# Kernel tuning notes

Hardware: AMD Instinct MI355X
Metric: run time of the kernel (lower is better)

The kernel has to match this reference:

```python
import jax, jax.numpy as jnp
import numpy as np

B, G, D, N_HEADS, FFN, L = 16, 2048, 256, 8, 1024, 4
HEAD_DIM = D // N_HEADS
EPS_LN = 1e-5
MASK_TOKEN = -10.0
REE_BASE = 100.0


def setup_inputs() -> dict:
    key = jax.random.key(0)
    ks = jax.random.split(key, 20)
    s = 0.02
    inp = {
        'x': jax.random.normal(ks[0], (B, G), jnp.float32),
        'gene_emb': jax.random.normal(ks[1], (G, D), jnp.float32) * s,
        'inv_freq': (1.0 / REE_BASE ** (jnp.arange(0, D, 2, dtype=jnp.float32) / D)),
        'Wq': jax.random.normal(ks[2], (L, D, D), jnp.float32) * s,
        'bq': jnp.zeros((L, D), jnp.float32),
        'Wk': jax.random.normal(ks[3], (L, D, D), jnp.float32) * s,
        'bk': jnp.zeros((L, D), jnp.float32),
        'Wv': jax.random.normal(ks[4], (L, D, D), jnp.float32) * s,
        'bv': jnp.zeros((L, D), jnp.float32),
        'ln1_g': jnp.ones((L, D), jnp.float32),
        'ln1_b': jnp.zeros((L, D), jnp.float32),
        'ln2_g': jnp.ones((L, D), jnp.float32),
        'ln2_b': jnp.zeros((L, D), jnp.float32),
        'WU': jax.random.normal(ks[5], (L, D, FFN), jnp.float32) * s,
        'bU': jnp.zeros((L, FFN), jnp.float32),
        'WV': jax.random.normal(ks[6], (L, FFN, D), jnp.float32) * s,
        'bV': jnp.zeros((L, D), jnp.float32),
        'Wout': jax.random.normal(ks[7], (D, 1), jnp.float32) * s,
        'bout': jnp.zeros((1,), jnp.float32),
    }
    return inp


def layernorm(x, g, b):
    m = x.mean(-1, keepdims=True)
    v = ((x - m) ** 2).mean(-1, keepdims=True)
    return (x - m) / jnp.sqrt(v + EPS_LN) * g + b


def causal_linear_attention(q, k, v):
    # q, k already feature-mapped ('sqr'); shapes [B, S, H, dh]
    b, s, h, dh = q.shape
    qs, ks_, vs = (jnp.moveaxis(t, 1, 0) for t in (q, k, v))  # [S,B,H,dh]
    num0 = jnp.zeros((b, h, dh, dh), q.dtype)
    den0 = jnp.zeros((b, h, dh), q.dtype)

    def step(carry, qkv):
        num_s, den_s = carry
        qt, kt, vt = qkv
        num_s = num_s + jnp.einsum('bhf,bhd->bhfd', kt, vt)
        den_s = den_s + kt
        num = jnp.einsum('bhf,bhfd->bhd', qt, num_s)
        den = jnp.einsum('bhf,bhf->bh', qt, den_s)
        return (num_s, den_s), num / (den[..., None] + 1e-16)

    _, out = jax.lax.scan(step, (num0, den0), (qs, ks_, vs))  # [S,B,H,dh]
    return jnp.moveaxis(out, 0, 1).reshape(b, s, h * dh)


def reference(x, gene_emb, inv_freq, Wq, bq, Wk, bk, Wv, bv,
              ln1_g, ln1_b, ln2_g, ln2_b, WU, bU, WV, bV, Wout, bout):
    b, g = x.shape
    # Rotary Expression Embedding
    freqs = x[..., None] * inv_freq  # [B,G,D/2]
    emb = jnp.concatenate([jnp.sin(freqs), jnp.cos(freqs)], axis=-1)  # [B,G,D]
    emb = jnp.where((x == MASK_TOKEN)[..., None], 0.0, emb)
    h = gene_emb[None] + emb  # [B,G,D]

    for l in range(Wq.shape[0]):
        hn = layernorm(h, ln1_g[l], ln1_b[l])  # pre-LN (on_gptln=True)
        q = (hn @ Wq[l] + bq[l]).reshape(b, g, N_HEADS, HEAD_DIM) ** 2
        k = (hn @ Wk[l] + bk[l]).reshape(b, g, N_HEADS, HEAD_DIM) ** 2
        v = (hn @ Wv[l] + bv[l]).reshape(b, g, N_HEADS, HEAD_DIM)
        h = h + causal_linear_attention(q, k, v)
        hn2 = layernorm(h, ln2_g[l], ln2_b[l])
        h = h + jax.nn.gelu(hn2 @ WU[l] + bU[l], approximate=False) @ WV[l] + bV[l]
    return (h @ Wout + bout).squeeze(-1)  # [B,G]
```

## Files before the change

kernel.cpp:

```cpp
#include <hip/hip_runtime.h>
#include <math.h>


#define GG 2048
#define DD 256
#define NROWS 32768
#define NC 32
#define CS 64

typedef __attribute__((ext_vector_type(8))) short bf16x8;
typedef __attribute__((ext_vector_type(4))) float f32x4;

__device__ __forceinline__ short f2bf(float f) {
  union { float f; unsigned u; } v; v.f = f;
  unsigned r = v.u + 0x7FFFu + ((v.u >> 16) & 1u);
  return (short)(r >> 16);
}
__device__ __forceinline__ float bf2f(short s) {
  union { unsigned u; float f; } v; v.u = ((unsigned)(unsigned short)s) << 16;
  return v.f;
}
__device__ __forceinline__ void gld16(const short* g, short* l) {
  __builtin_amdgcn_global_load_lds(
      (const __attribute__((address_space(1))) void*)g,
      (__attribute__((address_space(3))) void*)l, 16, 0, 0);
}
__device__ __forceinline__ float fast_gelu(float x) {
  float y = 1.595769122f * (x + 0.044715f * x * x * x);
  return x / (1.0f + __expf(-y));
}

__global__ __launch_bounds__(256) void embed_kernel(
    const float* __restrict__ x, const float* __restrict__ ge,
    const float* __restrict__ invf, float* __restrict__ h) {
  int bg = blockIdx.x * 4 + (threadIdx.x >> 6);
  int g = bg & (GG - 1);
  int lane = threadIdx.x & 63;
  float xv = x[bg];
  int d = lane * 4;
  float4 e;
  if (lane < 32) {
    float4 f = *(const float4*)&invf[d];
    e.x = sinf(xv * f.x); e.y = sinf(xv * f.y);
    e.z = sinf(xv * f.z); e.w = sinf(xv * f.w);
  } else {
    float4 f = *(const float4*)&invf[d - 128];
    e.x = cosf(xv * f.x); e.y = cosf(xv * f.y);
    e.z = cosf(xv * f.z); e.w = cosf(xv * f.w);
  }
  if (xv == -10.0f) { e.x = 0.f; e.y = 0.f; e.z = 0.f; e.w = 0.f; }
  float4 gv = *(const float4*)&ge[(size_t)g * DD + d];
  float4 o; o.x = gv.x + e.x; o.y = gv.y + e.y; o.z = gv.z + e.z; o.w = gv.w + e.w;
  *(float4*)&h[(size_t)bg * DD + d] = o;
}

__global__ __launch_bounds__(256) void ln_tiled(
    const float* __restrict__ h, const float* __restrict__ gamma,
    const float* __restrict__ beta, short* __restrict__ outT) {
  __shared__ float mean_s[32], rstd_s[32];
  __shared__ float gls[256], bls[256];
  int r0 = blockIdx.x * 32;
  int tid = threadIdx.x;
  gls[tid] = gamma[tid]; bls[tid] = beta[tid];
  {
    int row = tid >> 3, seg = tid & 7;
    const float4* hp = (const float4*)(h + (size_t)(r0 + row) * DD + seg * 32);
    float s = 0.f, s2 = 0.f;
#pragma unroll
    for (int i = 0; i < 8; ++i) {
      float4 v = hp[i];
      s += v.x + v.y + v.z + v.w;
      s2 += v.x * v.x + v.y * v.y + v.z * v.z + v.w * v.w;
    }
    s += __shfl_xor(s, 1); s += __shfl_xor(s, 2); s += __shfl_xor(s, 4);
    s2 += __shfl_xor(s2, 1); s2 += __shfl_xor(s2, 2); s2 += __shfl_xor(s2, 4);
    if (seg == 0) {
      float mn = s * (1.0f / 256.0f);
      mean_s[row] = mn;
      rstd_s[row] = rsqrtf(s2 * (1.0f / 256.0f) - mn * mn + 1e-5f);
    }
  }
  __syncthreads();
  int row = tid & 31, kc8 = (tid >> 5) & 3, half = tid >> 7;
  float mn = mean_s[row], rs = rstd_s[row];
  size_t hrow = (size_t)(r0 + row) * DD;
  int trow = (r0 & 127) + row;
  short* tb = outT + (size_t)(r0 >> 7) * 8 * 4096 + (kc8 * 128 + trow) * 8;
#pragma unroll
  for (int j = 0; j < 4; ++j) {
    int kb = half * 4 + j;
    int k0 = kb * 32 + kc8 * 8;
    float4 x0 = *(const float4*)&h[hrow + k0];
    float4 x1 = *(const float4*)&h[hrow + k0 + 4];
    float4 g0 = *(const float4*)&gls[k0], g1 = *(const float4*)&gls[k0 + 4];
    float4 b0 = *(const float4*)&bls[k0], b1 = *(const float4*)&bls[k0 + 4];
    bf16x8 aw;
    aw[0] = f2bf((x0.x - mn) * rs * g0.x + b0.x);
    aw[1] = f2bf((x0.y - mn) * rs * g0.y + b0.y);
    aw[2] = f2bf((x0.z - mn) * rs * g0.z + b0.z);
    aw[3] = f2bf((x0.w - mn) * rs * g0.w + b0.w);
    aw[4] = f2bf((x1.x - mn) * rs * g1.x + b1.x);
    aw[5] = f2bf((x1.y - mn) * rs * g1.y + b1.y);
    aw[6] = f2bf((x1.z - mn) * rs * g1.z + b1.z);
    aw[7] = f2bf((x1.w - mn) * rs * g1.w + b1.w);
    *(bf16x8*)&tb[(size_t)kb * 4096] = aw;
  }
}

__global__ __launch_bounds__(256) void prep_weights(
    const float* __restrict__ Wq, const float* __restrict__ Wk,
    const float* __restrict__ Wv, const float* __restrict__ WU,
    const float* __restrict__ WV,
    short* __restrict__ TQ, short* __restrict__ TK, short* __restrict__ TV,
    short* __restrict__ TU, short* __restrict__ TVd) {
  int zz = blockIdx.z, l = blockIdx.y;
  const float* src; short* dst; int Kd, Nd;
  if (zz == 0) { src = Wq; dst = TQ; Kd = 256; Nd = 256; }
  else if (zz == 1) { src = Wk; dst = TK; Kd = 256; Nd = 256; }
  else if (zz == 2) { src = Wv; dst = TV; Kd = 256; Nd = 256; }
  else if (zz == 3) { src = WU; dst = TU; Kd = 256; Nd = 1024; }
  else { src = WV; dst = TVd; Kd = 1024; Nd = 256; }
  int tot = Kd * Nd;
  int e = blockIdx.x * 256 + threadIdx.x;
  if (e >= tot) return;
  int t = e >> 12;
  int cslot = (e >> 3) & 511;
  int elem = e & 7;
  int kc8 = cslot >> 7, rn = cslot & 127;
  int nKb = Kd >> 5;
  int nt = t / nKb, kb = t - nt * nKb;
  int n = nt * 128 + rn, k = kb * 32 + kc8 * 8 + elem;
  dst[(size_t)l * tot + e] = f2bf(src[(size_t)l * tot + (size_t)k * Nd + n]);
}

template <int K, int EPI>
__global__ __launch_bounds__(256) void gemm_t(
    const short* __restrict__ A, const short* __restrict__ B0,
    const short* __restrict__ B1, const short* __restrict__ B2,
    const float* __restrict__ bias0, const float* __restrict__ bias1,
    const float* __restrict__ bias2,
    short* __restrict__ o0, short* __restrict__ o1, short* __restrict__ o2,
    float* __restrict__ outf, int N) {
  __shared__ __align__(16) short L[24576];
  constexpr int nIter = K / 32;
  int z = blockIdx.z;
  const short* Bt = (z == 0) ? B0 : (z == 1) ? B1 : B2;
  const float* bias = (z == 0) ? bias0 : (z == 1) ? bias1 : bias2;
  short* outz = (z == 0) ? o0 : (z == 1) ? o1 : o2;
  int m0 = blockIdx.x * 128, n0 = blockIdx.y * 128;
  int tid = threadIdx.x;
  int lane = tid & 63, w = tid >> 6;
  int q = lane >> 4, r = lane & 15;
  int wm = (w >> 1) * 64, wn = (w & 1) * 64;
  const short* At = A + (size_t)blockIdx.x * nIter * 4096;
  const short* Btl = Bt + (size_t)blockIdx.y * nIter * 4096;
  f32x4 vzero = {0.f, 0.f, 0.f, 0.f};
  f32x4 acc[4][4];
#pragma unroll
  for (int i = 0; i < 4; ++i)
#pragma unroll
    for (int j = 0; j < 4; ++j) acc[i][j] = vzero;

  int c0 = tid * 8, c1 = (tid + 256) * 8;
#pragma unroll
  for (int g = 0; g < 3; ++g) {
    gld16(At + g * 4096 + c0, &L[g * 4096 + c0]);
    gld16(At + g * 4096 + c1, &L[g * 4096 + c1]);
    gld16(Btl + g * 4096 + c0, &L[12288 + g * 4096 + c0]);
    gld16(Btl + g * 4096 + c1, &L[12288 + g * 4096 + c1]);
  }

  int abase = (q * 128 + wm + r) * 8;
  int bbase = (q * 128 + wn + r) * 8;

#pragma unroll
  for (int gi = 0; gi < nIter; ++gi) {
    const int rem = nIter - 1 - gi;
    if (rem >= 2)      __builtin_amdgcn_s_waitcnt(0x0f78);
    else if (rem == 1) __builtin_amdgcn_s_waitcnt(0x0f74);
    else               __builtin_amdgcn_s_waitcnt(0x0f70);
    __builtin_amdgcn_s_barrier();
    const int cur = gi % 3;
    const short* Asc = &L[cur * 4096];
    const short* Bsc = &L[12288 + cur * 4096];
    bf16x8 af[4], bfr[4];
#pragma unroll
    for (int mt = 0; mt < 4; ++mt)
      af[mt] = *(const bf16x8*)&Asc[abase + mt * 16 * 8];
#pragma unroll
    for (int nt = 0; nt < 4; ++nt)
      bfr[nt] = *(const bf16x8*)&Bsc[bbase + nt * 16 * 8];
#pragma unroll
    for (int mt = 0; mt < 4; ++mt)
#pragma unroll
      for (int nt = 0; nt < 4; ++nt)
        acc[mt][nt] = __builtin_amdgcn_mfma_f32_16x16x32_bf16(bfr[nt], af[mt], acc[mt][nt], 0, 0, 0);
    __builtin_amdgcn_s_waitcnt(0xc07f);
    __builtin_amdgcn_s_barrier();
    if (gi + 3 < nIter) {
      size_t kn = (size_t)(gi + 3) * 4096;
      gld16(At + kn + c0, &L[cur * 4096 + c0]);
      gld16(At + kn + c1, &L[cur * 4096 + c1]);
      gld16(Btl + kn + c0, &L[12288 + cur * 4096 + c0]);
      gld16(Btl + kn + c1, &L[12288 + cur * 4096 + c1]);
    }
  }

  float4 bias4[4];
#pragma unroll
  for (int nt = 0; nt < 4; ++nt) bias4[nt] = *(const float4*)&bias[n0 + wn + nt * 16 + q * 4];

  if (EPI == 0) {
    short* T = L;
#pragma unroll
    for (int mt = 0; mt < 4; ++mt) {
      int ml = wm + mt * 16 + r;
#pragma unroll
      for (int nt = 0; nt < 4; ++nt) {
        f32x4 v = acc[mt][nt];
        v[0] += bias4[nt].x; v[1] += bias4[nt].y; v[2] += bias4[nt].z; v[3] += bias4[nt].w;
        if (z < 2) { v[0] *= v[0]; v[1] *= v[1]; v[2] *= v[2]; v[3] *= v[3]; }
        short4 pk; pk.x = f2bf(v[0]); pk.y = f2bf(v[1]); pk.z = f2bf(v[2]); pk.w = f2bf(v[3]);
        *(short4*)&T[ml * 132 + wn + nt * 16 + q * 4] = pk;
      }
    }
    __syncthreads();
#pragma unroll
    for (int t2 = 0; t2 < 2; ++t2) {
      int task = tid + t2 * 256;
      int row = task & 127, hl = task >> 7;
      size_t obase = ((size_t)((n0 >> 5) + hl) * NROWS + m0 + row) * 32;
#pragma unroll
      for (int j = 0; j < 4; ++j)
        *(bf16x8*)&outz[obase + j * 8] = *(const bf16x8*)&T[row * 132 + hl * 32 + j * 8];
    }
  } else if (EPI == 1) {
#pragma unroll
    for (int mt = 0; mt < 4; ++mt) {
      int ml = wm + mt * 16 + r;
#pragma unroll
      for (int nt = 0; nt < 4; ++nt) {
        f32x4 v = acc[mt][nt];
        v[0] += bias4[nt].x; v[1] += bias4[nt].y; v[2] += bias4[nt].z; v[3] += bias4[nt].w;
#pragma unroll
        for (int e = 0; e < 4; ++e) v[e] = fast_gelu(v[e]);
        short4 o; o.x = f2bf(v[0]); o.y = f2bf(v[1]); o.z = f2bf(v[2]); o.w = f2bf(v[3]);
        int n = n0 + wn + nt * 16 + q * 4;
        size_t ti = ((size_t)blockIdx.x * (N >> 5) + (n >> 5)) * 4096 +
                    (size_t)(((n >> 3) & 3) << 10) + (ml << 3) + (n & 7);
        *(short4*)&outz[ti] = o;
      }
    }
  } else {
    float* TF = (float*)L;
#pragma unroll
    for (int half = 0; half < 2; ++half) {
      __syncthreads();
      if ((w & 1) == half) {
#pragma unroll
        for (int mt = 0; mt < 4; ++mt) {
          int ml = wm + mt * 16 + r;
#pragma unroll
          for (int nt = 0; nt < 4; ++nt) {
            f32x4 v = acc[mt][nt];
            v[0] += bias4[nt].x; v[1] += bias4[nt].y; v[2] += bias4[nt].z; v[3] += bias4[nt].w;
            *(f32x4*)&TF[ml * 68 + nt * 16 + q * 4] = v;
          }
        }
      }
      __syncthreads();
      int row = tid >> 1, col = (tid & 1) * 32;
      size_t hoff = (size_t)(m0 + row) * N + n0 + half * 64 + col;
#pragma unroll
      for (int j = 0; j < 8; ++j) {
        float4 add = *(const float4*)&TF[row * 68 + col + j * 4];
        float4 cur4 = *(float4*)&outf[hoff + j * 4];
        cur4.x += add.x; cur4.y += add.y; cur4.z += add.z; cur4.w += add.w;
        *(float4*)&outf[hoff + j * 4] = cur4;
      }
    }
  }
}

__global__ __launch_bounds__(256) void attn_chunk_kv(
    const short* __restrict__ Kb, const short* __restrict__ Vb,
    float* __restrict__ St, float* __restrict__ Zc) {
  __shared__ short Kt[4][32 * 72];
  __shared__ short Vt[4][32 * 72];
  int wid = threadIdx.x >> 6;
  int blk = blockIdx.x * 4 + wid;
  int c = blk & (NC - 1), bh = blk >> 5;
  int b = bh >> 3, hh = bh & 7;
  int lane = threadIdx.x & 63, q = lane >> 4, r = lane & 15;
  size_t rowbase = ((size_t)hh * NROWS + b * GG + c * CS + lane) * 32;
#pragma unroll
  for (int j = 0; j < 4; ++j) {
    bf16x8 kv = *(const bf16x8*)&Kb[rowbase + j * 8];
    bf16x8 vv = *(const bf16x8*)&Vb[rowbase + j * 8];
#pragma unroll
    for (int e = 0; e < 8; ++e) {
      Kt[wid][(j * 8 + e) * 72 + lane] = kv[e];
      Vt[wid][(j * 8 + e) * 72 + lane] = vv[e];
    }
  }
  __syncthreads();
  f32x4 vzero = {0.f, 0.f, 0.f, 0.f};
  f32x4 acc[2][2];
#pragma unroll
  for (int i = 0; i < 2; ++i)
#pragma unroll
    for (int j = 0; j < 2; ++j) acc[i][j] = vzero;
#pragma unroll
  for (int ks = 0; ks < 2; ++ks) {
    bf16x8 afr[2], bfr[2];
#pragma unroll
    for (int mt = 0; mt < 2; ++mt) afr[mt] = *(const bf16x8*)&Kt[wid][(mt * 16 + r) * 72 + ks * 32 + q * 8];
#pragma unroll
    for (int nt = 0; nt < 2; ++nt) bfr[nt] = *(const bf16x8*)&Vt[wid][(nt * 16 + r) * 72 + ks * 32 + q * 8];
#pragma unroll
    for (int mt = 0; mt < 2; ++mt)
#pragma unroll
      for (int nt = 0; nt < 2; ++nt)
        acc[mt][nt] = __builtin_amdgcn_mfma_f32_16x16x32_bf16(afr[mt], bfr[nt], acc[mt][nt], 0, 0, 0);
  }
  float* stp = St + ((size_t)bh * NC + c) * 1024;
#pragma unroll
  for (int mt = 0; mt < 2; ++mt)
#pragma unroll
    for (int nt = 0; nt < 2; ++nt)
      *(f32x4*)&stp[(nt * 16 + r) * 32 + mt * 16 + q * 4] = acc[mt][nt];
  if (lane < 32) {
    float s = 0.f;
#pragma unroll
    for (int j = 0; j < 8; ++j) {
      bf16x8 kr = *(const bf16x8*)&Kt[wid][lane * 72 + j * 8];
#pragma unroll
      for (int e = 0; e < 8; ++e) s += bf2f(kr[e]);
    }
    Zc[((size_t)bh * NC + c) * 32 + lane] = s;
  }
}

__global__ __launch_bounds__(1024) void attn_prefix(float* __restrict__ St, float* __restrict__ Zc) {
  int bh = blockIdx.x, i = threadIdx.x;
  float run = 0.f;
  float* p = St + (size_t)bh * NC * 1024 + i;
#pragma unroll
  for (int c = 0; c < NC; ++c) { float t = p[(size_t)c * 1024]; p[(size_t)c * 1024] = run; run += t; }
  if (i < 32) {
    float rz = 0.f;
    float* pz = Zc + (size_t)bh * NC * 32 + i;
#pragma unroll
    for (int c = 0; c < NC; ++c) { float t = pz[c * 32]; pz[c * 32] = rz; rz += t; }
  }
}

__global__ __launch_bounds__(256) void attn_intra(
    const short* __restrict__ Qb, const short* __restrict__ Kb,
    const short* __restrict__ Vb, const float* __restrict__ St,
    const float* __restrict__ Zc, float* __restrict__ h) {
  __shared__ short P[4][64 * 72];
  __shared__ short Vt[4][32 * 72];
  __shared__ float den[4][64];
  int wid = threadIdx.x >> 6;
  int blk = blockIdx.x * 4 + wid;
  int c = blk & (NC - 1), bh = blk >> 5;
  int b = bh >> 3, hh = bh & 7;
  int lane = threadIdx.x & 63, q = lane >> 4, r = lane & 15;
  size_t hrow0 = (size_t)b * GG + c * CS;
  size_t qrow0 = (size_t)hh * NROWS + b * GG + c * CS;

  const float* zp = Zc + ((size_t)bh * NC + c) * 32;
  float qz = 0.f;
  {
    size_t qoff = (qrow0 + lane) * 32;
#pragma unroll
    for (int j = 0; j < 4; ++j) {
      bf16x8 qv = *(const bf16x8*)&Qb[qoff + j * 8];
#pragma unroll
      for (int e = 0; e < 8; ++e) qz += bf2f(qv[e]) * zp[j * 8 + e];
    }
  }
  den[wid][lane] = qz;

  {
    size_t voff = (qrow0 + lane) * 32;
#pragma unroll
    for (int j = 0; j < 4; ++j) {
      bf16x8 vv = *(const bf16x8*)&Vb[voff + j * 8];
#pragma unroll
      for (int e = 0; e < 8; ++e) Vt[wid][(j * 8 + e) * 72 + lane] = vv[e];
    }
  }

  bf16x8 ak[4], bqf[4];
#pragma unroll
  for (int t4 = 0; t4 < 4; ++t4) {
    ak[t4]  = *(const bf16x8*)&Kb[(qrow0 + t4 * 16 + r) * 32 + q * 8];
    bqf[t4] = *(const bf16x8*)&Qb[(qrow0 + t4 * 16 + r) * 32 + q * 8];
  }
  f32x4 vzero = {0.f, 0.f, 0.f, 0.f};
  f32x4 pacc[4][4];
#pragma unroll
  for (int mt = 0; mt < 4; ++mt)
#pragma unroll
    for (int nt = 0; nt < 4; ++nt)
      pacc[mt][nt] = __builtin_amdgcn_mfma_f32_16x16x32_bf16(ak[mt], bqf[nt], vzero, 0, 0, 0);

  float rs[4] = {0.f, 0.f, 0.f, 0.f};
#pragma unroll
  for (int nt = 0; nt < 4; ++nt) {
    int t = nt * 16 + r;
#pragma unroll
    for (int mt = 0; mt < 4; ++mt) {
      short4 pk;
#pragma unroll
      for (int rr = 0; rr < 4; ++rr) {
        int s = mt * 16 + q * 4 + rr;
        float pv = (s <= t) ? pacc[mt][nt][rr] : 0.f;
        rs[nt] += pv;
        ((short*)&pk)[rr] = f2bf(pv);
      }
      *(short4*)&P[wid][t * 72 + mt * 16 + q * 4] = pk;
    }
  }
#pragma unroll
  for (int nt = 0; nt < 4; ++nt) {
    rs[nt] += __shfl_xor(rs[nt], 16);
    rs[nt] += __shfl_xor(rs[nt], 32);
  }
  __syncthreads();
  if (lane < 16) {
#pragma unroll
    for (int nt = 0; nt < 4; ++nt) den[wid][nt * 16 + lane] += rs[nt];
  }
  __syncthreads();

  f32x4 oacc[4][2];
#pragma unroll
  for (int mt = 0; mt < 4; ++mt)
#pragma unroll
    for (int nt2 = 0; nt2 < 2; ++nt2) oacc[mt][nt2] = vzero;
  const float* stp = St + ((size_t)bh * NC + c) * 1024;
#pragma unroll
  for (int nt2 = 0; nt2 < 2; ++nt2) {
    float4 s0 = *(const float4*)&stp[(nt2 * 16 + r) * 32 + q * 8];
    float4 s1 = *(const float4*)&stp[(nt2 * 16 + r) * 32 + q * 8 + 4];
    bf16x8 bs;
    bs[0] = f2bf(s0.x); bs[1] = f2bf(s0.y); bs[2] = f2bf(s0.z); bs[3] = f2bf(s0.w);
    bs[4] = f2bf(s1.x); bs[5] = f2bf(s1.y); bs[6] = f2bf(s1.z); bs[7] = f2bf(s1.w);
#pragma unroll
    for (int mt = 0; mt < 4; ++mt)
      oacc[mt][nt2] = __builtin_amdgcn_mfma_f32_16x16x32_bf16(bqf[mt], bs, oacc[mt][nt2], 0, 0, 0);
  }
#pragma unroll
  for (int ks = 0; ks < 2; ++ks) {
    bf16x8 ap[4];
#pragma unroll
    for (int mt = 0; mt < 4; ++mt)
      ap[mt] = *(const bf16x8*)&P[wid][(mt * 16 + r) * 72 + ks * 32 + q * 8];
#pragma unroll
    for (int nt2 = 0; nt2 < 2; ++nt2) {
      bf16x8 bv_ = *(const bf16x8*)&Vt[wid][(nt2 * 16 + r) * 72 + ks * 32 + q * 8];
#pragma unroll
      for (int mt = 0; mt < 4; ++mt)
        oacc[mt][nt2] = __builtin_amdgcn_mfma_f32_16x16x32_bf16(ap[mt], bv_, oacc[mt][nt2], 0, 0, 0);
    }
  }

#pragma unroll
  for (int mt = 0; mt < 4; ++mt) {
#pragma unroll
    for (int rr = 0; rr < 4; ++rr) {
      int t = mt * 16 + q * 4 + rr;
      float inv = 1.0f / (den[wid][t] + 1e-16f);
#pragma unroll
      for (int nt2 = 0; nt2 < 2; ++nt2) {
        int d = nt2 * 16 + r;
        size_t off = (hrow0 + t) * DD + hh * 32 + d;
        h[off] += oacc[mt][nt2][rr] * inv;
      }
    }
  }
}

__global__ __launch_bounds__(256) void out_proj(
    const float* __restrict__ h, const float* __restrict__ Wout,
    const float* __restrict__ bout, float* __restrict__ out) {
  int row = blockIdx.x * 4 + (threadIdx.x >> 6);
  int lane = threadIdx.x & 63;
  float4 a = *(const float4*)&h[(size_t)row * DD + lane * 4];
  float4 w = *(const float4*)&Wout[lane * 4];
  float s = a.x * w.x + a.y * w.y + a.z * w.z + a.w * w.w;
#pragma unroll
  for (int o = 1; o < 64; o <<= 1) s += __shfl_xor(s, o);
  if (lane == 0) out[row] = s + bout[0];
}

extern "C" void kernel_launch(void* const* d_in, const int* in_sizes, int n_in,
                              void* d_out, int out_size, void* d_ws, size_t ws_size,
                              hipStream_t stream) {
  const float* x    = (const float*)d_in[0];
  const float* ge   = (const float*)d_in[1];
  const float* invf = (const float*)d_in[2];
  const float* Wq   = (const float*)d_in[3];
  const float* bq   = (const float*)d_in[4];
  const float* Wk   = (const float*)d_in[5];
  const float* bk   = (const float*)d_in[6];
  const float* Wv   = (const float*)d_in[7];
  const float* bv   = (const float*)d_in[8];
  const float* ln1g = (const float*)d_in[9];
  const float* ln1b = (const float*)d_in[10];
  const float* ln2g = (const float*)d_in[11];
  const float* ln2b = (const float*)d_in[12];
  const float* WU   = (const float*)d_in[13];
  const float* bU   = (const float*)d_in[14];
  const float* WV   = (const float*)d_in[15];
  const float* bV   = (const float*)d_in[16];
  const float* Wout = (const float*)d_in[17];
  const float* bout = (const float*)d_in[18];
  float* out = (float*)d_out;

  char* ws = (char*)d_ws;
  float* h   = (float*)(ws + 0);
  short* hn  = (short*)(ws + 33554432);
  char*  R   = ws + 50331648;
  short* qb  = (short*)(R + 0);
  short* kb  = (short*)(R + 16777216);
  short* vb  = (short*)(R + 33554432);
  float* St  = (float*)(R + 50331648);
  float* Zc  = (float*)(R + 67108864);
  short* mid = (short*)(R + 0);
  char*  WT  = R + 67633152;
  short* TQ  = (short*)(WT + 0);
  short* TK  = (short*)(WT + 524288);
  short* TVq = (short*)(WT + 1048576);
  short* TU  = (short*)(WT + 1572864);
  short* TVd = (short*)(WT + 3670016);

  prep_weights<<<dim3(1024, 4, 5), 256, 0, stream>>>(Wq, Wk, Wv, WU, WV, TQ, TK, TVq, TU, TVd);
  embed_kernel<<<NROWS / 4, 256, 0, stream>>>(x, ge, invf, h);

  for (int l = 0; l < 4; ++l) {
    ln_tiled<<<NROWS / 32, 256, 0, stream>>>(h, ln1g + l * 256, ln1b + l * 256, hn);
    gemm_t<256, 0><<<dim3(256, 2, 3), 256, 0, stream>>>(
        hn, TQ + l * 65536, TK + l * 65536, TVq + l * 65536,
        bq + l * 256, bk + l * 256, bv + l * 256,
        qb, kb, vb, nullptr, 256);
    attn_chunk_kv<<<1024, 256, 0, stream>>>(kb, vb, St, Zc);
    attn_prefix<<<128, 1024, 0, stream>>>(St, Zc);
    attn_intra<<<1024, 256, 0, stream>>>(qb, kb, vb, St, Zc, h);
    ln_tiled<<<NROWS / 32, 256, 0, stream>>>(h, ln2g + l * 256, ln2b + l * 256, hn);
    gemm_t<256, 1><<<dim3(256, 8, 1), 256, 0, stream>>>(
        hn, TU + l * 262144, nullptr, nullptr,
        bU + l * 1024, nullptr, nullptr,
        mid, nullptr, nullptr, nullptr, 1024);
    gemm_t<1024, 2><<<dim3(256, 2, 1), 256, 0, stream>>>(
        mid, TVd + l * 262144, nullptr, nullptr,
        bV + l * 256, nullptr, nullptr,
        nullptr, nullptr, nullptr, h, 256);
  }
  out_proj<<<NROWS / 4, 256, 0, stream>>>(h, Wout, bout, out);
}
```

Baseline: 814.3 us.

## Fuse FFN up and down projections into a single LDS-resident kernel

```diff
diff --git a/kernel.cpp b/kernel.cpp
--- a/kernel.cpp
+++ b/kernel.cpp
@@ -10,6 +10,9 @@
 
 typedef __attribute__((ext_vector_type(8))) short bf16x8;
 typedef __attribute__((ext_vector_type(4))) float f32x4;
+
+struct FalseT { static constexpr bool value = false; };
+struct TrueT  { static constexpr bool value = true;  };
 
 __device__ __forceinline__ short f2bf(float f) {
   union { float f; unsigned u; } v; v.f = f;
@@ -282,6 +285,156 @@
   }
 }
 
+__global__ __launch_bounds__(512) void ffn_fused(
+    const short* __restrict__ A, const short* __restrict__ TUw,
+    const short* __restrict__ TVw, const float* __restrict__ bUp,
+    const float* __restrict__ bVp, float* __restrict__ h) {
+  __shared__ __align__(16) short L[75776];
+  float* BU = (float*)&L[73728];
+  int tid = threadIdx.x;
+  int lane = tid & 63, w = tid >> 6;
+  int q = lane >> 4, r = lane & 15;
+  int wmU = (w >> 2) * 64, wnU = (w & 3) * 32;
+  int wmD = (w >> 2) * 64, wnD = (w & 3) * 64;
+  int c16 = tid * 8;
+  const short* At = A + (size_t)blockIdx.x * 32768;
+
+  if (tid < 256) *(float4*)&BU[tid * 4] = *(const float4*)&bUp[tid * 4];
+
+#pragma unroll
+  for (int i = 0; i < 8; ++i) gld16(At + i * 4096 + c16, &L[i * 4096 + c16]);
+
+  auto issueUp = [&](int ss, int jj, int buf) {
+    short* dst = &L[49152 + buf * 8192];
+    const short* g0 = TUw + ((size_t)ss * 8 + jj * 2) * 4096;
+    gld16(g0 + c16, dst + c16);
+    gld16(g0 + 4096 + c16, dst + 4096 + c16);
+  };
+  auto issueDown = [&](int ss, int ii, int buf) {
+    short* dst = &L[49152 + buf * 8192];
+    gld16(TVw + (size_t)(ss * 4 + ii) * 4096 + c16, dst + c16);
+    gld16(TVw + (size_t)(32 + ss * 4 + ii) * 4096 + c16, dst + 4096 + c16);
+  };
+
+  issueUp(0, 0, 0); issueUp(0, 1, 1); issueUp(0, 2, 2);
+
+  f32x4 vzero = {0.f, 0.f, 0.f, 0.f};
+  f32x4 accm[4][2], acco[4][4];
+#pragma unroll
+  for (int mt = 0; mt < 4; ++mt) {
+#pragma unroll
+    for (int nt = 0; nt < 2; ++nt) accm[mt][nt] = vzero;
+#pragma unroll
+    for (int nt = 0; nt < 4; ++nt) acco[mt][nt] = vzero;
+  }
+
+  int cur = 0;
+
+  auto slice = [&](int s, auto lastc) {
+    constexpr bool LAST = decltype(lastc)::value;
+#pragma unroll
+    for (int j = 0; j < 4; ++j) {
+      __builtin_amdgcn_s_waitcnt(0x0f74);
+      __builtin_amdgcn_s_barrier();
+      const short* Ws = &L[49152 + cur * 8192];
+#pragma unroll
+      for (int kk = 0; kk < 2; ++kk) {
+        int kb = j * 2 + kk;
+        bf16x8 af[4], bfr[2];
+#pragma unroll
+        for (int mt = 0; mt < 4; ++mt)
+          af[mt] = *(const bf16x8*)&L[kb * 4096 + (q * 128 + wmU + mt * 16 + r) * 8];
+#pragma unroll
+        for (int nt = 0; nt < 2; ++nt)
+          bfr[nt] = *(const bf16x8*)&Ws[kk * 4096 + (q * 128 + wnU + nt * 16 + r) * 8];
+#pragma unroll
+        for (int mt = 0; mt < 4; ++mt)
+#pragma unroll
+          for (int nt = 0; nt < 2; ++nt)
+            accm[mt][nt] = __builtin_amdgcn_mfma_f32_16x16x32_bf16(bfr[nt], af[mt], accm[mt][nt], 0, 0, 0);
+      }
+      if (j == 3) {
+        float4 b4[2];
+#pragma unroll
+        for (int nt = 0; nt < 2; ++nt)
+          b4[nt] = *(const float4*)&BU[s * 128 + wnU + nt * 16 + q * 4];
+#pragma unroll
+        for (int mt = 0; mt < 4; ++mt) {
+          int row = wmU + mt * 16 + r;
+#pragma unroll
+          for (int nt = 0; nt < 2; ++nt) {
+            f32x4 v = accm[mt][nt];
+            v[0] += b4[nt].x; v[1] += b4[nt].y; v[2] += b4[nt].z; v[3] += b4[nt].w;
+            short4 pk;
+            pk.x = f2bf(fast_gelu(v[0])); pk.y = f2bf(fast_gelu(v[1]));
+            pk.z = f2bf(fast_gelu(v[2])); pk.w = f2bf(fast_gelu(v[3]));
+            int kc8 = 2 * nt + (q >> 1);
+            *(short4*)&L[32768 + (w & 3) * 4096 + (kc8 * 128 + row) * 8 + (q & 1) * 4] = pk;
+            accm[mt][nt] = vzero;
+          }
+        }
+      }
+      __builtin_amdgcn_s_waitcnt(0xc07f);
+      __builtin_amdgcn_s_barrier();
+      if (j == 0) issueUp(s, 3, cur);
+      else issueDown(s, j - 1, cur);
+      cur = (cur == 2) ? 0 : cur + 1;
+    }
+#pragma unroll
+    for (int i = 0; i < 4; ++i) {
+      if (LAST && i == 2)      __builtin_amdgcn_s_waitcnt(0x0f72);
+      else if (LAST && i == 3) __builtin_amdgcn_s_waitcnt(0x0f70);
+      else                     __builtin_amdgcn_s_waitcnt(0x0f74);
+      __builtin_amdgcn_s_barrier();
+      const short* Ws = &L[49152 + cur * 8192];
+      bf16x8 am[4], bvf[4];
+#pragma unroll
+      for (int mt = 0; mt < 4; ++mt)
+        am[mt] = *(const bf16x8*)&L[32768 + i * 4096 + (q * 128 + wmD + mt * 16 + r) * 8];
+#pragma unroll
+      for (int nt = 0; nt < 4; ++nt)
+        bvf[nt] = *(const bf16x8*)&Ws[(wnD >> 7) * 4096 + (q * 128 + (wnD & 127) + nt * 16 + r) * 8];
+#pragma unroll
+      for (int mt = 0; mt < 4; ++mt)
+#pragma unroll
+        for (int nt = 0; nt < 4; ++nt)
+          acco[mt][nt] = __builtin_amdgcn_mfma_f32_16x16x32_bf16(bvf[nt], am[mt], acco[mt][nt], 0, 0, 0);
+      __builtin_amdgcn_s_waitcnt(0xc07f);
+      __builtin_amdgcn_s_barrier();
+      if (i == 0) issueDown(s, 3, cur);
+      else if (!LAST) issueUp(s + 1, i - 1, cur);
+      cur = (cur == 2) ? 0 : cur + 1;
+    }
+  };
+
+  for (int s = 0; s < 7; ++s) slice(s, FalseT{});
+  slice(7, TrueT{});
+
+  float4 bv4[4];
+#pragma unroll
+  for (int nt = 0; nt < 4; ++nt) bv4[nt] = *(const float4*)&bVp[wnD + nt * 16 + q * 4];
+  float* TF = (float*)L;
+#pragma unroll
+  for (int mt = 0; mt < 4; ++mt) {
+    int row = wmD + mt * 16 + r;
+#pragma unroll
+    for (int nt = 0; nt < 4; ++nt) {
+      f32x4 v = acco[mt][nt];
+      v[0] += bv4[nt].x; v[1] += bv4[nt].y; v[2] += bv4[nt].z; v[3] += bv4[nt].w;
+      *(f32x4*)&TF[row * 260 + wnD + nt * 16 + q * 4] = v;
+    }
+  }
+  __syncthreads();
+  size_t hbase = ((size_t)blockIdx.x * 128 + w * 16) * DD;
+#pragma unroll
+  for (int j = 0; j < 16; ++j) {
+    float4 add = *(const float4*)&TF[(w * 16 + j) * 260 + lane * 4];
+    float4 c4 = *(float4*)&h[hbase + (size_t)j * DD + lane * 4];
+    c4.x += add.x; c4.y += add.y; c4.z += add.z; c4.w += add.w;
+    *(float4*)&h[hbase + (size_t)j * DD + lane * 4] = c4;
+  }
+}
+
 __global__ __launch_bounds__(256) void attn_chunk_kv(
     const short* __restrict__ Kb, const short* __restrict__ Vb,
     float* __restrict__ St, float* __restrict__ Zc) {
@@ -530,7 +683,6 @@
   short* vb  = (short*)(R + 33554432);
   float* St  = (float*)(R + 50331648);
   float* Zc  = (float*)(R + 67108864);
-  short* mid = (short*)(R + 0);
   char*  WT  = R + 67633152;
   short* TQ  = (short*)(WT + 0);
   short* TK  = (short*)(WT + 524288);
@@ -551,14 +703,8 @@
     attn_prefix<<<128, 1024, 0, stream>>>(St, Zc);
     attn_intra<<<1024, 256, 0, stream>>>(qb, kb, vb, St, Zc, h);
     ln_tiled<<<NROWS / 32, 256, 0, stream>>>(h, ln2g + l * 256, ln2b + l * 256, hn);
-    gemm_t<256, 1><<<dim3(256, 8, 1), 256, 0, stream>>>(
-        hn, TU + l * 262144, nullptr, nullptr,
-        bU + l * 1024, nullptr, nullptr,
-        mid, nullptr, nullptr, nullptr, 1024);
-    gemm_t<1024, 2><<<dim3(256, 2, 1), 256, 0, stream>>>(
-        mid, TVd + l * 262144, nullptr, nullptr,
-        bV + l * 256, nullptr, nullptr,
-        nullptr, nullptr, nullptr, h, 256);
+    ffn_fused<<<256, 512, 0, stream>>>(hn, TU + l * 262144, TVd + l * 262144,
+                                       bU + l * 1024, bV + l * 256, h);
   }
   out_proj<<<NROWS / 4, 256, 0, stream>>>(h, Wout, bout, out);
 }
```

Result: faster. 748.7 us (-8.0%).
